# Performance work log

Measured on AMD Instinct MI355X. Metric: run time of the kernel, lower is better.

Reference implementation:

```python
import jax, jax.numpy as jnp
import numpy as np
import math

D = 128
LAMBDA_INIT = 0.8 - 0.6 * math.exp(-0.3 * 1)  # depth=1


def _clin(xr, xi, wr, wi, br, bi):
    # complex linear: (xr + i xi) @ (wr + i wi)^T + (br + i bi)
    o_r = jnp.einsum('bhsd,od->bhso', xr, wr) - jnp.einsum('bhsd,od->bhso', xi, wi) + br
    o_i = jnp.einsum('bhsd,od->bhso', xr, wi) + jnp.einsum('bhsd,od->bhso', xi, wr) + bi
    return o_r, o_i


def setup_inputs() -> dict:
    key = jax.random.key(0)
    ks = jax.random.split(key, 32)
    B, H, S = 1, 12, 1024
    shp = (B, H, S, D)
    inp = {}
    names = ['q_r', 'q_i', 'k_r', 'k_i', 'v_r', 'v_i', 'pe_q_r', 'pe_q_i', 'pe_k_r', 'pe_k_i']
    for i, n in enumerate(names):
        inp[n] = jax.random.normal(ks[i], shp, dtype=jnp.float32)
    std = 1.0 / math.sqrt(D)
    inp['qw_r'] = jax.random.normal(ks[10], (2 * D, D), jnp.float32) * std
    inp['qw_i'] = jax.random.normal(ks[11], (2 * D, D), jnp.float32) * std
    inp['qb_r'] = jnp.zeros((2 * D,), jnp.float32)
    inp['qb_i'] = jnp.zeros((2 * D,), jnp.float32)
    for j, p in enumerate(['k', 'v', 'g', 'o']):
        inp[p + 'w_r'] = jax.random.normal(ks[12 + 2 * j], (D, D), jnp.float32) * std
        inp[p + 'w_i'] = jax.random.normal(ks[13 + 2 * j], (D, D), jnp.float32) * std
        inp[p + 'b_r'] = jnp.zeros((D,), jnp.float32)
        inp[p + 'b_i'] = jnp.zeros((D,), jnp.float32)
    inp['lq1'] = jax.random.normal(ks[20], (D,), jnp.float32) * 0.1
    inp['lk1'] = jax.random.normal(ks[21], (D,), jnp.float32) * 0.1
    inp['lq2'] = jax.random.normal(ks[22], (D,), jnp.float32) * 0.1
    inp['lk2'] = jax.random.normal(ks[23], (D,), jnp.float32) * 0.1
    inp['sub_w'] = jnp.ones((2 * D,), jnp.float32)
    return inp


def _forward(q_r, q_i, k_r, k_i, v_r, v_i, pe_q_r, pe_q_i, pe_k_r, pe_k_i,
             qw_r, qw_i, qb_r, qb_i, kw_r, kw_i, kb_r, kb_i,
             vw_r, vw_i, vb_r, vb_i, gw_r, gw_i, gb_r, gb_i,
             ow_r, ow_i, ob_r, ob_i, lq1, lk1, lq2, lk2, sub_w):
    scale = D ** (-0.5)
    qp_r, qp_i = _clin(q_r, q_i, qw_r, qw_i, qb_r, qb_i)   # [B,H,S,2D]
    kp_r, kp_i = _clin(k_r, k_i, kw_r, kw_i, kb_r, kb_i)   # [B,H,S,D]
    vp_r, vp_i = _clin(v_r, v_i, vw_r, vw_i, vb_r, vb_i)
    qp_r = qp_r + jnp.concatenate([pe_q_r, pe_q_r], axis=-1)
    qp_i = qp_i + jnp.concatenate([pe_q_i, pe_q_i], axis=-1)
    kp_r = kp_r + pe_k_r
    kp_i = kp_i + pe_k_i
    q1_r, q2_r = jnp.split(qp_r, 2, axis=-1)
    q1_i, q2_i = jnp.split(qp_i, 2, axis=-1)

    def attn_w(qr, qi):
        s_r = jnp.einsum('bhqd,bhkd->bhqk', qr, kp_r) + jnp.einsum('bhqd,bhkd->bhqk', qi, kp_i)
        s_i = jnp.einsum('bhqd,bhkd->bhqk', qi, kp_r) - jnp.einsum('bhqd,bhkd->bhqk', qr, kp_i)
        mag = jnp.sqrt(s_r ** 2 + s_i ** 2 + 1e-8) * scale
        return jax.nn.softmax(mag.astype(jnp.float32), axis=-1).astype(s_r.dtype)

    w1 = attn_w(q1_r, q1_i)
    w2 = attn_w(q2_r, q2_i)
    a1_r = jnp.einsum('bhqk,bhkd->bhqd', w1, vp_r)
    a1_i = jnp.einsum('bhqk,bhkd->bhqd', w1, vp_i)
    a2_r = jnp.einsum('bhqk,bhkd->bhqd', w2, vp_r)
    a2_i = jnp.einsum('bhqk,bhkd->bhqd', w2, vp_i)
    cat_r = jnp.concatenate([a1_r, a2_r], axis=-1)
    cat_i = jnp.concatenate([a1_i, a2_i], axis=-1)
    rms = jnp.sqrt(jnp.mean(cat_r ** 2 + cat_i ** 2, axis=-1, keepdims=True) + 1e-5)
    cat_r = cat_r / rms * sub_w
    cat_i = cat_i / rms * sub_w
    a1_r, a2_r = jnp.split(cat_r, 2, axis=-1)
    a1_i, a2_i = jnp.split(cat_i, 2, axis=-1)
    lam1 = jnp.exp(jnp.sum(lq1 * lk1))
    lam2 = jnp.exp(jnp.sum(lq2 * lk2))
    lam = jax.nn.sigmoid(lam1 - lam2 + LAMBDA_INIT)
    out_r = a1_r - lam * a2_r
    out_i = a1_i - lam * a2_i
    g_r, g_i = _clin(q_r, q_i, gw_r, gw_i, gb_r, gb_i)
    out_r, out_i = g_r * out_r - g_i * out_i, g_r * out_i + g_i * out_r
    out_r, out_i = _clin(out_r, out_i, ow_r, ow_i, ob_r, ob_i)
    return out_r, out_i


def reference(q_r, q_i, k_r, k_i, v_r, v_i, pe_q_r, pe_q_i, pe_k_r, pe_k_i,
              qw_r, qw_i, qb_r, qb_i, kw_r, kw_i, kb_r, kb_i,
              vw_r, vw_i, vb_r, vb_i, gw_r, gw_i, gb_r, gb_i,
              ow_r, ow_i, ob_r, ob_i, lq1, lk1, lq2, lk2, sub_w):
    return _forward(q_r, q_i, k_r, k_i, v_r, v_i, pe_q_r, pe_q_i, pe_k_r, pe_k_i,
                    qw_r, qw_i, qb_r, qb_i, kw_r, kw_i, kb_r, kb_i,
                    vw_r, vw_i, vb_r, vb_i, gw_r, gw_i, gb_r, gb_i,
                    ow_r, ow_i, ob_r, ob_i, lq1, lk1, lq2, lk2, sub_w)
```

## Files before the change

kernel.cpp:

```cpp
#include <hip/hip_runtime.h>
#include <math.h>

#define H 12
#define S 1024
#define D 128
#define NROWS (H * S)

typedef __attribute__((ext_vector_type(8))) _Float16 f16x8;
typedef __attribute__((ext_vector_type(4))) float f32x4;
typedef __attribute__((ext_vector_type(4))) int i32x4;

__device__ __forceinline__ short f2h(float f) {
    _Float16 h = (_Float16)f;
    return __builtin_bit_cast(short, h);
}
__device__ __forceinline__ float h2f(short s) {
    return (float)__builtin_bit_cast(_Float16, s);
}
__device__ __forceinline__ f16x8 fneg8(f16x8 v) {
    i32x4 u = __builtin_bit_cast(i32x4, v);
    u ^= (int)0x80008000;
    return __builtin_bit_cast(f16x8, u);
}

#define WS_QP_R   0ULL
#define WS_QP_I   6291456ULL
#define WS_KP_R   12582912ULL
#define WS_KP_I   15728640ULL
#define WS_VPT_R  18874368ULL
#define WS_VPT_I  22020096ULL
#define WS_GP_R   25165824ULL
#define WS_GP_I   28311552ULL
#define WS_ACAT_R 31457280ULL
#define WS_ACAT_I 37748736ULL
#define WS_LAM    44040192ULL
#define WS_SC     44040448ULL
#define W16_PER_HEAD   4194304ULL
#define STAT_PER_HEAD  16384ULL

__global__ void lam_kernel(const float* __restrict__ lq1, const float* __restrict__ lk1,
                           const float* __restrict__ lq2, const float* __restrict__ lk2,
                           float* __restrict__ lam_out)
{
    int t = threadIdx.x;
    float p1 = lq1[t] * lk1[t];
    float p2 = lq2[t] * lk2[t];
    #pragma unroll
    for (int off = 32; off; off >>= 1) {
        p1 += __shfl_xor(p1, off);
        p2 += __shfl_xor(p2, off);
    }
    __shared__ float s1[2], s2[2];
    if ((t & 63) == 0) { s1[t >> 6] = p1; s2[t >> 6] = p2; }
    __syncthreads();
    if (t == 0) {
        float l1 = expf(s1[0] + s1[1]);
        float l2 = expf(s2[0] + s2[1]);
        float x = l1 - l2 + 0.3555090675909693f;
        lam_out[0] = 1.0f / (1.0f + expf(-x));
    }
}

__global__ __launch_bounds__(256) void proj_all(
    const float* __restrict__ q_r, const float* __restrict__ q_i,
    const float* __restrict__ k_r, const float* __restrict__ k_i,
    const float* __restrict__ v_r, const float* __restrict__ v_i,
    const float* __restrict__ pe_q_r, const float* __restrict__ pe_q_i,
    const float* __restrict__ pe_k_r, const float* __restrict__ pe_k_i,
    const float* __restrict__ qw_r, const float* __restrict__ qw_i,
    const float* __restrict__ qb_r, const float* __restrict__ qb_i,
    const float* __restrict__ kw_r, const float* __restrict__ kw_i,
// ... 153 lines not shown
        for (int ks = 0; ks < 64; ks += 32) {
            f16x8 bfr[2], bfi[2];
            #pragma unroll
            for (int j = 0; j < 2; ++j) {
                bfr[j] = *(const f16x8*)&Brs[(wn + j * 16 + fm) * 72 + ks + fq * 8];
                bfi[j] = *(const f16x8*)&Bis[(wn + j * 16 + fm) * 72 + ks + fq * 8];
            }
            #pragma unroll
            for (int i = 0; i < 2; ++i) {
                f16x8 a = *(const f16x8*)&As[(wm + i * 16 + fm) * 72 + ks + fq * 8];
                #pragma unroll
                for (int j = 0; j < 2; ++j) {
                    accr[i][j] = __builtin_amdgcn_mfma_f32_16x16x32_f16(a, bfr[j], accr[i][j], 0, 0, 0);
                    acci[i][j] = __builtin_amdgcn_mfma_f32_16x16x32_f16(a, bfi[j], acci[i][j], 0, 0, 0);
                }
            }
        }
    }
    #pragma unroll
    for (int i = 0; i < 2; ++i)
        #pragma unroll
        for (int j = 0; j < 2; ++j) {
            int colc = col0 + wn + j * 16 + fm;
            float bbr = br[colc], bbi = bi[colc];
            #pragma unroll
            for (int reg = 0; reg < 4; ++reg) {
                int rr = row0 + wm + i * 16 + fq * 4 + reg;
                outr[(size_t)rr * 128 + colc] = accr[i][j][reg] + bbr;
                outi[(size_t)rr * 128 + colc] = acci[i][j][reg] + bbi;
            }
        }
}

__global__ __launch_bounds__(256) void score_mfma(
    const short* __restrict__ qp_r, const short* __restrict__ qp_i,
    const short* __restrict__ kp_r, const short* __restrict__ kp_i,
    short* __restrict__ w16, int h0)
{
    __shared__ short Qr[64 * 72], Qi[64 * 72], Kt[128 * 72];
    const int t = threadIdx.x;
    const int hh = blockIdx.z >> 1, map = blockIdx.z & 1;
    const int h = h0 + hh;
    const int q0 = blockIdx.x * 64, c0 = blockIdx.y * 128;
    const int lane = t & 63, wid = t >> 6;
    const int wm = (wid >> 1) * 32, wn = (wid & 1) * 64;
    const int fm = lane & 15, fq = lane >> 4;
    f32x4 zero4 = {0.f, 0.f, 0.f, 0.f};
    f32x4 sr[2][4], si[2][4];
    #pragma unroll
    for (int i = 0; i < 2; ++i)
        #pragma unroll
        for (int j = 0; j < 4; ++j) { sr[i][j] = zero4; si[i][j] = zero4; }

    for (int kb = 0; kb < 2; ++kb) {
        const int kbase = map * 128 + kb * 64;
        __syncthreads();
        #pragma unroll
        for (int i = 0; i < 4; ++i) {
            int lin = i * 256 + t;
            int r = lin >> 4, k4 = (lin & 15) * 4;
            size_t qb = (size_t)(h * S + q0 + r) * 256 + kbase + k4;
            *(short4*)&Qr[r * 72 + k4] = *(const short4*)&qp_r[qb];
            *(short4*)&Qi[r * 72 + k4] = *(const short4*)&qp_i[qb];
        }
        #pragma unroll
        for (int i = 0; i < 8; ++i) {
            int lin = i * 256 + t;
            int r = lin >> 4, k4 = (lin & 15) * 4;
            *(short4*)&Kt[r * 72 + k4] =
                *(const short4*)&kp_r[(size_t)(h * S + c0 + r) * 128 + kb * 64 + k4];
        }
        __syncthreads();
        f16x8 aR[2][2], aI[2][2];
        #pragma unroll
        for (int ks = 0; ks < 2; ++ks)
            #pragma unroll
            for (int i = 0; i < 2; ++i) {
                int ao = (wm + i * 16 + fm) * 72 + ks * 32 + fq * 8;
                aR[ks][i] = *(const f16x8*)&Qr[ao];
                aI[ks][i] = *(const f16x8*)&Qi[ao];
            }
        #pragma unroll
        for (int ks = 0; ks < 2; ++ks) {
            f16x8 b[4];
            #pragma unroll
            for (int j = 0; j < 4; ++j)
                b[j] = *(const f16x8*)&Kt[(wn + j * 16 + fm) * 72 + ks * 32 + fq * 8];
            #pragma unroll
            for (int i = 0; i < 2; ++i)
                #pragma unroll
                for (int j = 0; j < 4; ++j) {
                    sr[i][j] = __builtin_amdgcn_mfma_f32_16x16x32_f16(aR[ks][i], b[j], sr[i][j], 0, 0, 0);
                    si[i][j] = __builtin_amdgcn_mfma_f32_16x16x32_f16(aI[ks][i], b[j], si[i][j], 0, 0, 0);
                }
        }
        __syncthreads();
        #pragma unroll
        for (int i = 0; i < 8; ++i) {
            int lin = i * 256 + t;
            int r = lin >> 4, k4 = (lin & 15) * 4;
            *(short4*)&Kt[r * 72 + k4] =
                *(const short4*)&kp_i[(size_t)(h * S + c0 + r) * 128 + kb * 64 + k4];
        }
        __syncthreads();
        #pragma unroll
        for (int ks = 0; ks < 2; ++ks) {
            f16x8 b[4];
            #pragma unroll
            for (int j = 0; j < 4; ++j)
                b[j] = *(const f16x8*)&Kt[(wn + j * 16 + fm) * 72 + ks * 32 + fq * 8];
            f16x8 nR0 = fneg8(aR[ks][0]), nR1 = fneg8(aR[ks][1]);
            #pragma unroll
            for (int j = 0; j < 4; ++j) {
                sr[0][j] = __builtin_amdgcn_mfma_f32_16x16x32_f16(aI[ks][0], b[j], sr[0][j], 0, 0, 0);
                si[0][j] = __builtin_amdgcn_mfma_f32_16x16x32_f16(nR0, b[j], si[0][j], 0, 0, 0);
                sr[1][j] = __builtin_amdgcn_mfma_f32_16x16x32_f16(aI[ks][1], b[j], sr[1][j], 0, 0, 0);
                si[1][j] = __builtin_amdgcn_mfma_f32_16x16x32_f16(nR1, b[j], si[1][j], 0, 0, 0);
            }
        }
    }
    const float scale = 0.08838834764831845f;
    #pragma unroll
    for (int i = 0; i < 2; ++i)
        #pragma unroll
        for (int j = 0; j < 4; ++j) {
            int kcol = c0 + wn + j * 16 + fm;
            #pragma unroll
            for (int reg = 0; reg < 4; ++reg) {
                int q = q0 + wm + i * 16 + fq * 4 + reg;
                float r1 = sr[i][j][reg], I1 = si[i][j][reg];
                float m1 = sqrtf(fmaf(r1, r1, fmaf(I1, I1, 1e-8f))) * scale;
                w16[(((size_t)hh * 2 + map) * S + q) * S + kcol] = f2h(m1);
            }
        }
}

__global__ __launch_bounds__(256) void smstats(const short* __restrict__ w16,
                                               float2* __restrict__ stats)
{
    const short* row = w16 + (size_t)blockIdx.x * S;
    int t = threadIdx.x;
    short4 s = ((const short4*)row)[t];
    float f0 = h2f(s.x), f1 = h2f(s.y), f2v = h2f(s.z), f3 = h2f(s.w);
    float m = fmaxf(fmaxf(f0, f1), fmaxf(f2v, f3));
    #pragma unroll
    for (int off = 32; off; off >>= 1) m = fmaxf(m, __shfl_xor(m, off));
    __shared__ float redm[4], reds[4];
    int w = t >> 6;
    if ((t & 63) == 0) redm[w] = m;
    __syncthreads();
    m = fmaxf(fmaxf(redm[0], redm[1]), fmaxf(redm[2], redm[3]));
    float ssum = __expf(f0 - m) + __expf(f1 - m) + __expf(f2v - m) + __expf(f3 - m);
    #pragma unroll
    for (int off = 32; off; off >>= 1) ssum += __shfl_xor(ssum, off);
    if ((t & 63) == 0) reds[w] = ssum;
    __syncthreads();
    if (t == 0) {
        float total = reds[0] + reds[1] + reds[2] + reds[3];
        stats[blockIdx.x] = make_float2(m, 1.0f / total);
    }
}

__global__ __launch_bounds__(256) void av_mfma(
    const short* __restrict__ w16, const float2* __restrict__ stats,
    const short* __restrict__ vpT_r, const short* __restrict__ vpT_i,
    short* __restrict__ acat_r, short* __restrict__ acat_i, int h0)
{
    __shared__ short W1[32 * 72], W2[32 * 72], Vc[128 * 72];
    const int t = threadIdx.x;
    const int hh = blockIdx.z, h = h0 + hh;
    const int comp = blockIdx.y;
    const int q0 = blockIdx.x * 32;
    const short* vpT = comp ? vpT_i : vpT_r;
    short* acat = comp ? acat_i : acat_r;
    const float2* st1 = stats + ((size_t)hh * 2 + 0) * S;
    const float2* st2 = stats + ((size_t)hh * 2 + 1) * S;
    const int lane = t & 63, wid = t >> 6;
    const int wm = (wid >> 1) * 16, wn = (wid & 1) * 64;
    const int fm = lane & 15, fq = lane >> 4;
    f32x4 zero4 = {0.f, 0.f, 0.f, 0.f};
    f32x4 a1[4], a2[4];
    #pragma unroll
    for (int j = 0; j < 4; ++j) { a1[j] = zero4; a2[j] = zero4; }

    for (int k0 = 0; k0 < S; k0 += 64) {
        __syncthreads();
        #pragma unroll
        for (int it = 0; it < 2; ++it) {
            int lin = it * 256 + t;
            int r = lin >> 4, k4 = (lin & 15) * 4;
            float2 s1v = st1[q0 + r];
            float2 s2v = st2[q0 + r];
            short4 m1 = *(const short4*)&w16[(((size_t)hh * 2 + 0) * S + q0 + r) * S + k0 + k4];
            short4 m2 = *(const short4*)&w16[(((size_t)hh * 2 + 1) * S + q0 + r) * S + k0 + k4];
            *(short4*)&W1[r * 72 + k4] = make_short4(
                f2h(__expf(h2f(m1.x) - s1v.x) * s1v.y), f2h(__expf(h2f(m1.y) - s1v.x) * s1v.y),
                f2h(__expf(h2f(m1.z) - s1v.x) * s1v.y), f2h(__expf(h2f(m1.w) - s1v.x) * s1v.y));
            *(short4*)&W2[r * 72 + k4] = make_short4(
                f2h(__expf(h2f(m2.x) - s2v.x) * s2v.y), f2h(__expf(h2f(m2.y) - s2v.x) * s2v.y),
                f2h(__expf(h2f(m2.z) - s2v.x) * s2v.y), f2h(__expf(h2f(m2.w) - s2v.x) * s2v.y));
        }
        #pragma unroll
        for (int it = 0; it < 8; ++it) {
            int lin = it * 256 + t;
            int dd = lin >> 4, k4 = (lin & 15) * 4;
            *(short4*)&Vc[dd * 72 + k4] = *(const short4*)&vpT[(size_t)(h * 128 + dd) * 1024 + k0 + k4];
        }
        __syncthreads();
        #pragma unroll
        for (int ks = 0; ks < 64; ks += 32) {
            f16x8 b[4];
            #pragma unroll
            for (int j = 0; j < 4; ++j)
                b[j] = *(const f16x8*)&Vc[(wn + j * 16 + fm) * 72 + ks + fq * 8];
            int wo = (wm + fm) * 72 + ks + fq * 8;
            f16x8 w1f = *(const f16x8*)&W1[wo];
            f16x8 w2f = *(const f16x8*)&W2[wo];
            #pragma unroll
            for (int j = 0; j < 4; ++j) {
                a1[j] = __builtin_amdgcn_mfma_f32_16x16x32_f16(w1f, b[j], a1[j], 0, 0, 0);
                a2[j] = __builtin_amdgcn_mfma_f32_16x16x32_f16(w2f, b[j], a2[j], 0, 0, 0);
            }
        }
    }
    #pragma unroll
    for (int j = 0; j < 4; ++j) {
        int d = wn + j * 16 + fm;
        #pragma unroll
        for (int reg = 0; reg < 4; ++reg) {
            int q = q0 + wm + fq * 4 + reg;
            size_t rowb = (size_t)(h * S + q) * 256;
            acat[rowb + d]       = f2h(a1[j][reg]);
            acat[rowb + 128 + d] = f2h(a2[j][reg]);
        }
    }
}

__global__ __launch_bounds__(256) void rmsgate_kernel(
    const short* __restrict__ acat_r, const short* __restrict__ acat_i,
    const float* __restrict__ sub_w, const float* __restrict__ lam_ptr,
    short* __restrict__ gp_r, short* __restrict__ gp_i)
{
    int row = blockIdx.x;
    int t = threadIdx.x;
    float ar = h2f(acat_r[(size_t)row * 256 + t]);
    float ai = h2f(acat_i[(size_t)row * 256 + t]);
    float ss = fmaf(ar, ar, ai * ai);
    #pragma unroll
    for (int off = 32; off; off >>= 1) ss += __shfl_xor(ss, off);
    __shared__ float red[4];
    if ((t & 63) == 0) red[t >> 6] = ss;
    __syncthreads();
    float total = red[0] + red[1] + red[2] + red[3];
    float inv_rms = 1.0f / sqrtf(total * (1.0f / 256.0f) + 1e-5f);
    float sw = sub_w[t];
    __shared__ float Cr[256], Ci[256];
    Cr[t] = ar * inv_rms * sw;
    Ci[t] = ai * inv_rms * sw;
    __syncthreads();
    if (t < 128) {
        float lam = lam_ptr[0];
        float o_r = Cr[t] - lam * Cr[t + 128];
        float o_i = Ci[t] - lam * Ci[t + 128];
        float gr = h2f(gp_r[(size_t)row * 128 + t]);
        float gi = h2f(gp_i[(size_t)row * 128 + t]);
        gp_r[(size_t)row * 128 + t] = f2h(gr * o_r - gi * o_i);
        gp_i[(size_t)row * 128 + t] = f2h(gr * o_i + gi * o_r);
    }
}

extern "C" void kernel_launch(void* const* d_in, const int* in_sizes, int n_in,
                              void* d_out, int out_size, void* d_ws, size_t ws_size,
                              hipStream_t stream)
{
    (void)in_sizes; (void)n_in; (void)out_size;
    const float* q_r    = (const float*)d_in[0];
    const float* q_i    = (const float*)d_in[1];
    const float* k_r    = (const float*)d_in[2];
    const float* k_i    = (const float*)d_in[3];
    const float* v_r    = (const float*)d_in[4];
    const float* v_i    = (const float*)d_in[5];
    const float* pe_q_r = (const float*)d_in[6];
    const float* pe_q_i = (const float*)d_in[7];
    const float* pe_k_r = (const float*)d_in[8];
    const float* pe_k_i = (const float*)d_in[9];
    const float* qw_r   = (const float*)d_in[10];
    const float* qw_i   = (const float*)d_in[11];
    const float* qb_r   = (const float*)d_in[12];
    const float* qb_i   = (const float*)d_in[13];
    const float* kw_r   = (const float*)d_in[14];
    const float* kw_i   = (const float*)d_in[15];
    const float* kb_r   = (const float*)d_in[16];
    const float* kb_i   = (const float*)d_in[17];
    const float* vw_r   = (const float*)d_in[18];
    const float* vw_i   = (const float*)d_in[19];
    const float* vb_r   = (const float*)d_in[20];
    const float* vb_i   = (const float*)d_in[21];
    const float* gw_r   = (const float*)d_in[22];
    const float* gw_i   = (const float*)d_in[23];
    const float* gb_r   = (const float*)d_in[24];
    const float* gb_i   = (const float*)d_in[25];
    const float* ow_r   = (const float*)d_in[26];
    const float* ow_i   = (const float*)d_in[27];
    const float* ob_r   = (const float*)d_in[28];
    const float* ob_i   = (const float*)d_in[29];
    const float* lq1    = (const float*)d_in[30];
    const float* lk1    = (const float*)d_in[31];
    const float* lq2    = (const float*)d_in[32];
    const float* lk2    = (const float*)d_in[33];
    const float* sub_w  = (const float*)d_in[34];

    char* ws = (char*)d_ws;
    short* qp_r   = (short*)(ws + WS_QP_R);
    short* qp_i   = (short*)(ws + WS_QP_I);
    short* kp_r   = (short*)(ws + WS_KP_R);
    short* kp_i   = (short*)(ws + WS_KP_I);
    short* vpT_r  = (short*)(ws + WS_VPT_R);
    short* vpT_i  = (short*)(ws + WS_VPT_I);
    short* gp_r   = (short*)(ws + WS_GP_R);
    short* gp_i   = (short*)(ws + WS_GP_I);
    short* acat_r = (short*)(ws + WS_ACAT_R);
    short* acat_i = (short*)(ws + WS_ACAT_I);
    float* lam    = (float*)(ws + WS_LAM);
    short* w16    = (short*)(ws + WS_SC);

    float* out_r = (float*)d_out;
    float* out_i = out_r + (size_t)NROWS * D;

    size_t avail = ws_size > WS_SC ? ws_size - WS_SC : 0;
    int nh_chunk = (int)(avail / (W16_PER_HEAD + STAT_PER_HEAD));
    if (nh_chunk < 1) nh_chunk = 1;
    if (nh_chunk > H) nh_chunk = H;
    float2* stats = (float2*)(ws + WS_SC + (size_t)nh_chunk * W16_PER_HEAD);

    lam_kernel<<<1, 128, 0, stream>>>(lq1, lk1, lq2, lk2, lam);

    proj_all<<<dim3(192, 10), 256, 0, stream>>>(
        q_r, q_i, k_r, k_i, v_r, v_i, pe_q_r, pe_q_i, pe_k_r, pe_k_i,
        qw_r, qw_i, qb_r, qb_i, kw_r, kw_i, kb_r, kb_i,
        vw_r, vw_i, vb_r, vb_i, gw_r, gw_i, gb_r, gb_i,
        qp_r, qp_i, kp_r, kp_i, vpT_r, vpT_i, gp_r, gp_i);

    for (int h0 = 0; h0 < H; h0 += nh_chunk) {
        int nhh = (H - h0 < nh_chunk) ? (H - h0) : nh_chunk;
        score_mfma<<<dim3(16, 8, nhh * 2), 256, 0, stream>>>(qp_r, qp_i, kp_r, kp_i, w16, h0);
        smstats<<<nhh * 2 * S, 256, 0, stream>>>(w16, stats);
        av_mfma<<<dim3(32, 2, nhh), 256, 0, stream>>>(w16, stats, vpT_r, vpT_i, acat_r, acat_i, h0);
    }

    rmsgate_kernel<<<NROWS, 256, 0, stream>>>(acat_r, acat_i, sub_w, lam, gp_r, gp_i);

    oproj_mfma<<<dim3(192, 2), 256, 0, stream>>>(gp_r, gp_i, ow_r, ow_i, ob_r, ob_i, out_r, out_i);
}
```

Measured before the change: 296.7 us.

## Fuse score, softmax stats and AV into a flash-style attention kernel

```diff
diff --git a/kernel.cpp b/kernel.cpp
--- a/kernel.cpp
+++ b/kernel.cpp
@@ -34,9 +34,6 @@
 #define WS_ACAT_R 31457280ULL
 #define WS_ACAT_I 37748736ULL
 #define WS_LAM    44040192ULL
-#define WS_SC     44040448ULL
-#define W16_PER_HEAD   4194304ULL
-#define STAT_PER_HEAD  16384ULL
 
 __global__ void lam_kernel(const float* __restrict__ lq1, const float* __restrict__ lk1,
                            const float* __restrict__ lq2, const float* __restrict__ lk2,
@@ -256,206 +253,143 @@
         }
 }
 
-__global__ __launch_bounds__(256) void score_mfma(
+#define KI_OFF 8704
+#define VI_OFF 9216
+__global__ __launch_bounds__(128) void fused_attn(
     const short* __restrict__ qp_r, const short* __restrict__ qp_i,
     const short* __restrict__ kp_r, const short* __restrict__ kp_i,
-    short* __restrict__ w16, int h0)
+    const short* __restrict__ vpT_r, const short* __restrict__ vpT_i,
+    short* __restrict__ acat_r, short* __restrict__ acat_i)
 {
-    __shared__ short Qr[64 * 72], Qi[64 * 72], Kt[128 * 72];
+    __shared__ __align__(16) short KV[18432];
+    __shared__ __align__(16) short Pl[32 * 72];
     const int t = threadIdx.x;
-    const int hh = blockIdx.z >> 1, map = blockIdx.z & 1;
-    const int h = h0 + hh;
-    const int q0 = blockIdx.x * 64, c0 = blockIdx.y * 128;
     const int lane = t & 63, wid = t >> 6;
-    const int wm = (wid >> 1) * 32, wn = (wid & 1) * 64;
     const int fm = lane & 15, fq = lane >> 4;
+    const int q0 = blockIdx.x * 32;
+    const int map = blockIdx.y;
+    const int h = blockIdx.z;
+
+    f16x8 qR[4], qI[4];
+    {
+        size_t qrow = (size_t)(h * S + q0 + wid * 16 + fm) * 256 + map * 128;
+        #pragma unroll
+        for (int ks = 0; ks < 4; ++ks) {
+            qR[ks] = *(const f16x8*)&qp_r[qrow + ks * 32 + fq * 8];
+            qI[ks] = *(const f16x8*)&qp_i[qrow + ks * 32 + fq * 8];
+        }
+    }
     f32x4 zero4 = {0.f, 0.f, 0.f, 0.f};
-    f32x4 sr[2][4], si[2][4];
-    #pragma unroll
-    for (int i = 0; i < 2; ++i)
-        #pragma unroll
-        for (int j = 0; j < 4; ++j) { sr[i][j] = zero4; si[i][j] = zero4; }
-
-    for (int kb = 0; kb < 2; ++kb) {
-        const int kbase = map * 128 + kb * 64;
-        __syncthreads();
-        #pragma unroll
-        for (int i = 0; i < 4; ++i) {
-            int lin = i * 256 + t;
-            int r = lin >> 4, k4 = (lin & 15) * 4;
-            size_t qb = (size_t)(h * S + q0 + r) * 256 + kbase + k4;
-            *(short4*)&Qr[r * 72 + k4] = *(const short4*)&qp_r[qb];
-            *(short4*)&Qi[r * 72 + k4] = *(const short4*)&qp_i[qb];
-        }
-        #pragma unroll
-        for (int i = 0; i < 8; ++i) {
-            int lin = i * 256 + t;
-            int r = lin >> 4, k4 = (lin & 15) * 4;
-            *(short4*)&Kt[r * 72 + k4] =
-                *(const short4*)&kp_r[(size_t)(h * S + c0 + r) * 128 + kb * 64 + k4];
-        }
-        __syncthreads();
-        f16x8 aR[2][2], aI[2][2];
-        #pragma unroll
-        for (int ks = 0; ks < 2; ++ks)
-            #pragma unroll
-            for (int i = 0; i < 2; ++i) {
-                int ao = (wm + i * 16 + fm) * 72 + ks * 32 + fq * 8;
-                aR[ks][i] = *(const f16x8*)&Qr[ao];
-                aI[ks][i] = *(const f16x8*)&Qi[ao];
-            }
-        #pragma unroll
-        for (int ks = 0; ks < 2; ++ks) {
-            f16x8 b[4];
-            #pragma unroll
-            for (int j = 0; j < 4; ++j)
-                b[j] = *(const f16x8*)&Kt[(wn + j * 16 + fm) * 72 + ks * 32 + fq * 8];
-            #pragma unroll
-            for (int i = 0; i < 2; ++i)
+    f32x4 accO[2][8];
+    #pragma unroll
+    for (int c = 0; c < 2; ++c)
+        #pragma unroll
+        for (int dj = 0; dj < 8; ++dj) accO[c][dj] = zero4;
+    float m_run[4], l_run[4];
+    #pragma unroll
+    for (int reg = 0; reg < 4; ++reg) { m_run[reg] = -3.0e38f; l_run[reg] = 0.f; }
+
+    const float scale = 0.08838834764831845f;
+
+    for (int k0 = 0; k0 < S; k0 += 64) {
+        __syncthreads();
+        #pragma unroll
+        for (int it = 0; it < 8; ++it) {
+            int lin = it * 128 + t;
+            int r = lin >> 4, c8 = (lin & 15) * 8;
+            size_t src = (size_t)(h * S + k0 + r) * 128 + c8;
+            *(i32x4*)&KV[r * 136 + c8]          = *(const i32x4*)&kp_r[src];
+            *(i32x4*)&KV[KI_OFF + r * 136 + c8] = *(const i32x4*)&kp_i[src];
+        }
+        __syncthreads();
+        f32x4 sr[4], si[4];
+        #pragma unroll
+        for (int j = 0; j < 4; ++j) { sr[j] = zero4; si[j] = zero4; }
+        #pragma unroll
+        for (int ks = 0; ks < 4; ++ks) {
+            f16x8 aR = qR[ks], aI = qI[ks], nR = fneg8(qR[ks]);
+            #pragma unroll
+            for (int j = 0; j < 4; ++j) {
+                int bo = (j * 16 + fm) * 136 + ks * 32 + fq * 8;
+                f16x8 bR = *(const f16x8*)&KV[bo];
+                f16x8 bI = *(const f16x8*)&KV[KI_OFF + bo];
+                sr[j] = __builtin_amdgcn_mfma_f32_16x16x32_f16(aR, bR, sr[j], 0, 0, 0);
+                si[j] = __builtin_amdgcn_mfma_f32_16x16x32_f16(aI, bR, si[j], 0, 0, 0);
+                sr[j] = __builtin_amdgcn_mfma_f32_16x16x32_f16(aI, bI, sr[j], 0, 0, 0);
+                si[j] = __builtin_amdgcn_mfma_f32_16x16x32_f16(nR, bI, si[j], 0, 0, 0);
+            }
+        }
+        float p[4][4];
+        #pragma unroll
+        for (int j = 0; j < 4; ++j)
+            #pragma unroll
+            for (int reg = 0; reg < 4; ++reg)
+                p[j][reg] = sqrtf(fmaf(sr[j][reg], sr[j][reg],
+                                       fmaf(si[j][reg], si[j][reg], 1e-8f))) * scale;
+        float sc[4];
+        #pragma unroll
+        for (int reg = 0; reg < 4; ++reg) {
+            float mx = fmaxf(fmaxf(p[0][reg], p[1][reg]), fmaxf(p[2][reg], p[3][reg]));
+            #pragma unroll
+            for (int off = 1; off < 16; off <<= 1) mx = fmaxf(mx, __shfl_xor(mx, off));
+            float mnew = fmaxf(m_run[reg], mx);
+            sc[reg] = __expf(m_run[reg] - mnew);
+            m_run[reg] = mnew;
+            float ssum = 0.f;
+            #pragma unroll
+            for (int j = 0; j < 4; ++j) {
+                p[j][reg] = __expf(p[j][reg] - mnew);
+                ssum += p[j][reg];
+            }
+            #pragma unroll
+            for (int off = 1; off < 16; off <<= 1) ssum += __shfl_xor(ssum, off);
+            l_run[reg] = l_run[reg] * sc[reg] + ssum;
+        }
+        #pragma unroll
+        for (int c = 0; c < 2; ++c)
+            #pragma unroll
+            for (int dj = 0; dj < 8; ++dj)
                 #pragma unroll
-                for (int j = 0; j < 4; ++j) {
-                    sr[i][j] = __builtin_amdgcn_mfma_f32_16x16x32_f16(aR[ks][i], b[j], sr[i][j], 0, 0, 0);
-                    si[i][j] = __builtin_amdgcn_mfma_f32_16x16x32_f16(aI[ks][i], b[j], si[i][j], 0, 0, 0);
-                }
-        }
-        __syncthreads();
-        #pragma unroll
-        for (int i = 0; i < 8; ++i) {
-            int lin = i * 256 + t;
-            int r = lin >> 4, k4 = (lin & 15) * 4;
-            *(short4*)&Kt[r * 72 + k4] =
-                *(const short4*)&kp_i[(size_t)(h * S + c0 + r) * 128 + kb * 64 + k4];
-        }
-        __syncthreads();
-        #pragma unroll
-        for (int ks = 0; ks < 2; ++ks) {
-            f16x8 b[4];
-            #pragma unroll
-            for (int j = 0; j < 4; ++j)
-                b[j] = *(const f16x8*)&Kt[(wn + j * 16 + fm) * 72 + ks * 32 + fq * 8];
-            f16x8 nR0 = fneg8(aR[ks][0]), nR1 = fneg8(aR[ks][1]);
-            #pragma unroll
-            for (int j = 0; j < 4; ++j) {
-                sr[0][j] = __builtin_amdgcn_mfma_f32_16x16x32_f16(aI[ks][0], b[j], sr[0][j], 0, 0, 0);
-                si[0][j] = __builtin_amdgcn_mfma_f32_16x16x32_f16(nR0, b[j], si[0][j], 0, 0, 0);
-                sr[1][j] = __builtin_amdgcn_mfma_f32_16x16x32_f16(aI[ks][1], b[j], sr[1][j], 0, 0, 0);
-                si[1][j] = __builtin_amdgcn_mfma_f32_16x16x32_f16(nR1, b[j], si[1][j], 0, 0, 0);
-            }
-        }
-    }
-    const float scale = 0.08838834764831845f;
-    #pragma unroll
-    for (int i = 0; i < 2; ++i)
-        #pragma unroll
-        for (int j = 0; j < 4; ++j) {
-            int kcol = c0 + wn + j * 16 + fm;
-            #pragma unroll
-            for (int reg = 0; reg < 4; ++reg) {
-                int q = q0 + wm + i * 16 + fq * 4 + reg;
-                float r1 = sr[i][j][reg], I1 = si[i][j][reg];
-                float m1 = sqrtf(fmaf(r1, r1, fmaf(I1, I1, 1e-8f))) * scale;
-                w16[(((size_t)hh * 2 + map) * S + q) * S + kcol] = f2h(m1);
-            }
-        }
-}
-
-__global__ __launch_bounds__(256) void smstats(const short* __restrict__ w16,
-                                               float2* __restrict__ stats)
-{
-    const short* row = w16 + (size_t)blockIdx.x * S;
-    int t = threadIdx.x;
-    short4 s = ((const short4*)row)[t];
-    float f0 = h2f(s.x), f1 = h2f(s.y), f2v = h2f(s.z), f3 = h2f(s.w);
-    float m = fmaxf(fmaxf(f0, f1), fmaxf(f2v, f3));
-    #pragma unroll
-    for (int off = 32; off; off >>= 1) m = fmaxf(m, __shfl_xor(m, off));
-    __shared__ float redm[4], reds[4];
-    int w = t >> 6;
-    if ((t & 63) == 0) redm[w] = m;
-    __syncthreads();
-    m = fmaxf(fmaxf(redm[0], redm[1]), fmaxf(redm[2], redm[3]));
-    float ssum = __expf(f0 - m) + __expf(f1 - m) + __expf(f2v - m) + __expf(f3 - m);
-    #pragma unroll
-    for (int off = 32; off; off >>= 1) ssum += __shfl_xor(ssum, off);
-    if ((t & 63) == 0) reds[w] = ssum;
-    __syncthreads();
-    if (t == 0) {
-        float total = reds[0] + reds[1] + reds[2] + reds[3];
-        stats[blockIdx.x] = make_float2(m, 1.0f / total);
-    }
-}
-
-__global__ __launch_bounds__(256) void av_mfma(
-    const short* __restrict__ w16, const float2* __restrict__ stats,
-    const short* __restrict__ vpT_r, const short* __restrict__ vpT_i,
-    short* __restrict__ acat_r, short* __restrict__ acat_i, int h0)
-{
-    __shared__ short W1[32 * 72], W2[32 * 72], Vc[128 * 72];
-    const int t = threadIdx.x;
-    const int hh = blockIdx.z, h = h0 + hh;
-    const int comp = blockIdx.y;
-    const int q0 = blockIdx.x * 32;
-    const short* vpT = comp ? vpT_i : vpT_r;
-    short* acat = comp ? acat_i : acat_r;
-    const float2* st1 = stats + ((size_t)hh * 2 + 0) * S;
-    const float2* st2 = stats + ((size_t)hh * 2 + 1) * S;
-    const int lane = t & 63, wid = t >> 6;
-    const int wm = (wid >> 1) * 16, wn = (wid & 1) * 64;
-    const int fm = lane & 15, fq = lane >> 4;
-    f32x4 zero4 = {0.f, 0.f, 0.f, 0.f};
-    f32x4 a1[4], a2[4];
-    #pragma unroll
-    for (int j = 0; j < 4; ++j) { a1[j] = zero4; a2[j] = zero4; }
-
-    for (int k0 = 0; k0 < S; k0 += 64) {
-        __syncthreads();
-        #pragma unroll
-        for (int it = 0; it < 2; ++it) {
-            int lin = it * 256 + t;
-            int r = lin >> 4, k4 = (lin & 15) * 4;
-            float2 s1v = st1[q0 + r];
-            float2 s2v = st2[q0 + r];
-            short4 m1 = *(const short4*)&w16[(((size_t)hh * 2 + 0) * S + q0 + r) * S + k0 + k4];
-            short4 m2 = *(const short4*)&w16[(((size_t)hh * 2 + 1) * S + q0 + r) * S + k0 + k4];
-            *(short4*)&W1[r * 72 + k4] = make_short4(
-                f2h(__expf(h2f(m1.x) - s1v.x) * s1v.y), f2h(__expf(h2f(m1.y) - s1v.x) * s1v.y),
-                f2h(__expf(h2f(m1.z) - s1v.x) * s1v.y), f2h(__expf(h2f(m1.w) - s1v.x) * s1v.y));
-            *(short4*)&W2[r * 72 + k4] = make_short4(
-                f2h(__expf(h2f(m2.x) - s2v.x) * s2v.y), f2h(__expf(h2f(m2.y) - s2v.x) * s2v.y),
-                f2h(__expf(h2f(m2.z) - s2v.x) * s2v.y), f2h(__expf(h2f(m2.w) - s2v.x) * s2v.y));
-        }
+                for (int reg = 0; reg < 4; ++reg)
+                    accO[c][dj][reg] *= sc[reg];
+        __syncthreads();
         #pragma unroll
         for (int it = 0; it < 8; ++it) {
-            int lin = it * 256 + t;
-            int dd = lin >> 4, k4 = (lin & 15) * 4;
-            *(short4*)&Vc[dd * 72 + k4] = *(const short4*)&vpT[(size_t)(h * 128 + dd) * 1024 + k0 + k4];
-        }
-        __syncthreads();
-        #pragma unroll
-        for (int ks = 0; ks < 64; ks += 32) {
-            f16x8 b[4];
-            #pragma unroll
-            for (int j = 0; j < 4; ++j)
-                b[j] = *(const f16x8*)&Vc[(wn + j * 16 + fm) * 72 + ks + fq * 8];
-            int wo = (wm + fm) * 72 + ks + fq * 8;
-            f16x8 w1f = *(const f16x8*)&W1[wo];
-            f16x8 w2f = *(const f16x8*)&W2[wo];
-            #pragma unroll
-            for (int j = 0; j < 4; ++j) {
-                a1[j] = __builtin_amdgcn_mfma_f32_16x16x32_f16(w1f, b[j], a1[j], 0, 0, 0);
-                a2[j] = __builtin_amdgcn_mfma_f32_16x16x32_f16(w2f, b[j], a2[j], 0, 0, 0);
-            }
-        }
-    }
-    #pragma unroll
-    for (int j = 0; j < 4; ++j) {
-        int d = wn + j * 16 + fm;
-        #pragma unroll
-        for (int reg = 0; reg < 4; ++reg) {
-            int q = q0 + wm + fq * 4 + reg;
-            size_t rowb = (size_t)(h * S + q) * 256;
-            acat[rowb + d]       = f2h(a1[j][reg]);
-            acat[rowb + 128 + d] = f2h(a2[j][reg]);
+            int lin = it * 128 + t;
+            int dd = lin >> 3, c8 = (lin & 7) * 8;
+            size_t src = (size_t)(h * 128 + dd) * 1024 + k0 + c8;
+            *(i32x4*)&KV[dd * 72 + c8]          = *(const i32x4*)&vpT_r[src];
+            *(i32x4*)&KV[VI_OFF + dd * 72 + c8] = *(const i32x4*)&vpT_i[src];
+        }
+        #pragma unroll
+        for (int j = 0; j < 4; ++j)
+            #pragma unroll
+            for (int reg = 0; reg < 4; ++reg)
+                Pl[(wid * 16 + fq * 4 + reg) * 72 + j * 16 + fm] = f2h(p[j][reg]);
+        __syncthreads();
+        #pragma unroll
+        for (int ks2 = 0; ks2 < 2; ++ks2) {
+            f16x8 w8 = *(const f16x8*)&Pl[(wid * 16 + fm) * 72 + ks2 * 32 + fq * 8];
+            #pragma unroll
+            for (int dj = 0; dj < 8; ++dj) {
+                int vo = (dj * 16 + fm) * 72 + ks2 * 32 + fq * 8;
+                f16x8 br = *(const f16x8*)&KV[vo];
+                f16x8 bi = *(const f16x8*)&KV[VI_OFF + vo];
+                accO[0][dj] = __builtin_amdgcn_mfma_f32_16x16x32_f16(w8, br, accO[0][dj], 0, 0, 0);
+                accO[1][dj] = __builtin_amdgcn_mfma_f32_16x16x32_f16(w8, bi, accO[1][dj], 0, 0, 0);
+            }
+        }
+    }
+    #pragma unroll
+    for (int reg = 0; reg < 4; ++reg) {
+        float invl = 1.0f / l_run[reg];
+        int q = q0 + wid * 16 + fq * 4 + reg;
+        size_t rowb = (size_t)(h * S + q) * 256 + map * 128;
+        #pragma unroll
+        for (int dj = 0; dj < 8; ++dj) {
+            int d = dj * 16 + fm;
+            acat_r[rowb + d] = f2h(accO[0][dj][reg] * invl);
+            acat_i[rowb + d] = f2h(accO[1][dj][reg] * invl);
         }
     }
 }
@@ -497,7 +431,7 @@
                               void* d_out, int out_size, void* d_ws, size_t ws_size,
                               hipStream_t stream)
 {
-    (void)in_sizes; (void)n_in; (void)out_size;
+    (void)in_sizes; (void)n_in; (void)out_size; (void)ws_size;
     const float* q_r    = (const float*)d_in[0];
     const float* q_i    = (const float*)d_in[1];
     const float* k_r    = (const float*)d_in[2];
@@ -546,16 +480,9 @@
     short* acat_r = (short*)(ws + WS_ACAT_R);
     short* acat_i = (short*)(ws + WS_ACAT_I);
     float* lam    = (float*)(ws + WS_LAM);
-    short* w16    = (short*)(ws + WS_SC);
 
     float* out_r = (float*)d_out;
     float* out_i = out_r + (size_t)NROWS * D;
-
-    size_t avail = ws_size > WS_SC ? ws_size - WS_SC : 0;
-    int nh_chunk = (int)(avail / (W16_PER_HEAD + STAT_PER_HEAD));
-    if (nh_chunk < 1) nh_chunk = 1;
-    if (nh_chunk > H) nh_chunk = H;
-    float2* stats = (float2*)(ws + WS_SC + (size_t)nh_chunk * W16_PER_HEAD);
 
     lam_kernel<<<1, 128, 0, stream>>>(lq1, lk1, lq2, lk2, lam);
 
@@ -565,12 +492,8 @@
         vw_r, vw_i, vb_r, vb_i, gw_r, gw_i, gb_r, gb_i,
         qp_r, qp_i, kp_r, kp_i, vpT_r, vpT_i, gp_r, gp_i);
 
-    for (int h0 = 0; h0 < H; h0 += nh_chunk) {
-        int nhh = (H - h0 < nh_chunk) ? (H - h0) : nh_chunk;
-        score_mfma<<<dim3(16, 8, nhh * 2), 256, 0, stream>>>(qp_r, qp_i, kp_r, kp_i, w16, h0);
-        smstats<<<nhh * 2 * S, 256, 0, stream>>>(w16, stats);
-        av_mfma<<<dim3(32, 2, nhh), 256, 0, stream>>>(w16, stats, vpT_r, vpT_i, acat_r, acat_i, h0);
-    }
+    fused_attn<<<dim3(32, 2, H), 128, 0, stream>>>(
+        qp_r, qp_i, kp_r, kp_i, vpT_r, vpT_i, acat_r, acat_i);
 
     rmsgate_kernel<<<NROWS, 256, 0, stream>>>(acat_r, acat_i, sub_w, lam, gp_r, gp_i);
 
```

After: 575.3 us. +93.9%, slower.

## Fuse softmax stats into AV kernel via online softmax; load Q fragments directly

Applied to the files above, without the earlier changes.

```diff
diff --git a/kernel.cpp b/kernel.cpp
--- a/kernel.cpp
+++ b/kernel.cpp
@@ -36,7 +36,6 @@
 #define WS_LAM    44040192ULL
 #define WS_SC     44040448ULL
 #define W16_PER_HEAD   4194304ULL
-#define STAT_PER_HEAD  16384ULL
 
 __global__ void lam_kernel(const float* __restrict__ lq1, const float* __restrict__ lk1,
                            const float* __restrict__ lq2, const float* __restrict__ lk2,
@@ -261,7 +260,7 @@
     const short* __restrict__ kp_r, const short* __restrict__ kp_i,
     short* __restrict__ w16, int h0)
 {
-    __shared__ short Qr[64 * 72], Qi[64 * 72], Kt[128 * 72];
+    __shared__ short Kr[128 * 72], Ki[128 * 72];
     const int t = threadIdx.x;
     const int hh = blockIdx.z >> 1, map = blockIdx.z & 1;
     const int h = h0 + hh;
@@ -277,69 +276,42 @@
         for (int j = 0; j < 4; ++j) { sr[i][j] = zero4; si[i][j] = zero4; }
 
     for (int kb = 0; kb < 2; ++kb) {
-        const int kbase = map * 128 + kb * 64;
         __syncthreads();
         #pragma unroll
         for (int i = 0; i < 4; ++i) {
             int lin = i * 256 + t;
-            int r = lin >> 4, k4 = (lin & 15) * 4;
-            size_t qb = (size_t)(h * S + q0 + r) * 256 + kbase + k4;
-            *(short4*)&Qr[r * 72 + k4] = *(const short4*)&qp_r[qb];
-            *(short4*)&Qi[r * 72 + k4] = *(const short4*)&qp_i[qb];
-        }
-        #pragma unroll
-        for (int i = 0; i < 8; ++i) {
-            int lin = i * 256 + t;
-            int r = lin >> 4, k4 = (lin & 15) * 4;
-            *(short4*)&Kt[r * 72 + k4] =
-                *(const short4*)&kp_r[(size_t)(h * S + c0 + r) * 128 + kb * 64 + k4];
-        }
-        __syncthreads();
+            int r = lin >> 3, c8 = (lin & 7) * 8;
+            size_t src = (size_t)(h * S + c0 + r) * 128 + kb * 64 + c8;
+            *(i32x4*)&Kr[r * 72 + c8] = *(const i32x4*)&kp_r[src];
+            *(i32x4*)&Ki[r * 72 + c8] = *(const i32x4*)&kp_i[src];
+        }
         f16x8 aR[2][2], aI[2][2];
         #pragma unroll
         for (int ks = 0; ks < 2; ++ks)
             #pragma unroll
             for (int i = 0; i < 2; ++i) {
-                int ao = (wm + i * 16 + fm) * 72 + ks * 32 + fq * 8;
-                aR[ks][i] = *(const f16x8*)&Qr[ao];
-                aI[ks][i] = *(const f16x8*)&Qi[ao];
-            }
+                size_t qa = (size_t)(h * S + q0 + wm + i * 16 + fm) * 256
+                            + map * 128 + kb * 64 + ks * 32 + fq * 8;
+                aR[ks][i] = *(const f16x8*)&qp_r[qa];
+                aI[ks][i] = *(const f16x8*)&qp_i[qa];
+            }
+        __syncthreads();
         #pragma unroll
         for (int ks = 0; ks < 2; ++ks) {
-            f16x8 b[4];
-            #pragma unroll
-            for (int j = 0; j < 4; ++j)
-                b[j] = *(const f16x8*)&Kt[(wn + j * 16 + fm) * 72 + ks * 32 + fq * 8];
-            #pragma unroll
-            for (int i = 0; i < 2; ++i)
-                #pragma unroll
-                for (int j = 0; j < 4; ++j) {
-                    sr[i][j] = __builtin_amdgcn_mfma_f32_16x16x32_f16(aR[ks][i], b[j], sr[i][j], 0, 0, 0);
-                    si[i][j] = __builtin_amdgcn_mfma_f32_16x16x32_f16(aI[ks][i], b[j], si[i][j], 0, 0, 0);
-                }
-        }
-        __syncthreads();
-        #pragma unroll
-        for (int i = 0; i < 8; ++i) {
-            int lin = i * 256 + t;
-            int r = lin >> 4, k4 = (lin & 15) * 4;
-            *(short4*)&Kt[r * 72 + k4] =
-                *(const short4*)&kp_i[(size_t)(h * S + c0 + r) * 128 + kb * 64 + k4];
-        }
-        __syncthreads();
-        #pragma unroll
-        for (int ks = 0; ks < 2; ++ks) {
-            f16x8 b[4];
-            #pragma unroll
-            for (int j = 0; j < 4; ++j)
-                b[j] = *(const f16x8*)&Kt[(wn + j * 16 + fm) * 72 + ks * 32 + fq * 8];
             f16x8 nR0 = fneg8(aR[ks][0]), nR1 = fneg8(aR[ks][1]);
             #pragma unroll
             for (int j = 0; j < 4; ++j) {
-                sr[0][j] = __builtin_amdgcn_mfma_f32_16x16x32_f16(aI[ks][0], b[j], sr[0][j], 0, 0, 0);
-                si[0][j] = __builtin_amdgcn_mfma_f32_16x16x32_f16(nR0, b[j], si[0][j], 0, 0, 0);
-                sr[1][j] = __builtin_amdgcn_mfma_f32_16x16x32_f16(aI[ks][1], b[j], sr[1][j], 0, 0, 0);
-                si[1][j] = __builtin_amdgcn_mfma_f32_16x16x32_f16(nR1, b[j], si[1][j], 0, 0, 0);
+                int bo = (wn + j * 16 + fm) * 72 + ks * 32 + fq * 8;
+                f16x8 bR = *(const f16x8*)&Kr[bo];
+                f16x8 bI = *(const f16x8*)&Ki[bo];
+                sr[0][j] = __builtin_amdgcn_mfma_f32_16x16x32_f16(aR[ks][0], bR, sr[0][j], 0, 0, 0);
+                si[0][j] = __builtin_amdgcn_mfma_f32_16x16x32_f16(aI[ks][0], bR, si[0][j], 0, 0, 0);
+                sr[0][j] = __builtin_amdgcn_mfma_f32_16x16x32_f16(aI[ks][0], bI, sr[0][j], 0, 0, 0);
+                si[0][j] = __builtin_amdgcn_mfma_f32_16x16x32_f16(nR0, bI, si[0][j], 0, 0, 0);
+                sr[1][j] = __builtin_amdgcn_mfma_f32_16x16x32_f16(aR[ks][1], bR, sr[1][j], 0, 0, 0);
+                si[1][j] = __builtin_amdgcn_mfma_f32_16x16x32_f16(aI[ks][1], bR, si[1][j], 0, 0, 0);
+                sr[1][j] = __builtin_amdgcn_mfma_f32_16x16x32_f16(aI[ks][1], bI, sr[1][j], 0, 0, 0);
+                si[1][j] = __builtin_amdgcn_mfma_f32_16x16x32_f16(nR1, bI, si[1][j], 0, 0, 0);
             }
         }
     }
@@ -359,46 +331,19 @@
         }
 }
 
-__global__ __launch_bounds__(256) void smstats(const short* __restrict__ w16,
-                                               float2* __restrict__ stats)
-{
-    const short* row = w16 + (size_t)blockIdx.x * S;
-    int t = threadIdx.x;
-    short4 s = ((const short4*)row)[t];
-    float f0 = h2f(s.x), f1 = h2f(s.y), f2v = h2f(s.z), f3 = h2f(s.w);
-    float m = fmaxf(fmaxf(f0, f1), fmaxf(f2v, f3));
-    #pragma unroll
-    for (int off = 32; off; off >>= 1) m = fmaxf(m, __shfl_xor(m, off));
-    __shared__ float redm[4], reds[4];
-    int w = t >> 6;
-    if ((t & 63) == 0) redm[w] = m;
-    __syncthreads();
-    m = fmaxf(fmaxf(redm[0], redm[1]), fmaxf(redm[2], redm[3]));
-    float ssum = __expf(f0 - m) + __expf(f1 - m) + __expf(f2v - m) + __expf(f3 - m);
-    #pragma unroll
-    for (int off = 32; off; off >>= 1) ssum += __shfl_xor(ssum, off);
-    if ((t & 63) == 0) reds[w] = ssum;
-    __syncthreads();
-    if (t == 0) {
-        float total = reds[0] + reds[1] + reds[2] + reds[3];
-        stats[blockIdx.x] = make_float2(m, 1.0f / total);
-    }
-}
-
-__global__ __launch_bounds__(256) void av_mfma(
-    const short* __restrict__ w16, const float2* __restrict__ stats,
+__global__ __launch_bounds__(256) void av_online(
+    const short* __restrict__ w16,
     const short* __restrict__ vpT_r, const short* __restrict__ vpT_i,
     short* __restrict__ acat_r, short* __restrict__ acat_i, int h0)
 {
     __shared__ short W1[32 * 72], W2[32 * 72], Vc[128 * 72];
+    __shared__ float mrun[2][32], lrun[2][32], scL[2][32];
     const int t = threadIdx.x;
     const int hh = blockIdx.z, h = h0 + hh;
     const int comp = blockIdx.y;
     const int q0 = blockIdx.x * 32;
     const short* vpT = comp ? vpT_i : vpT_r;
     short* acat = comp ? acat_i : acat_r;
-    const float2* st1 = stats + ((size_t)hh * 2 + 0) * S;
-    const float2* st2 = stats + ((size_t)hh * 2 + 1) * S;
     const int lane = t & 63, wid = t >> 6;
     const int wm = (wid >> 1) * 16, wn = (wid & 1) * 64;
     const int fm = lane & 15, fq = lane >> 4;
@@ -406,6 +351,10 @@
     f32x4 a1[4], a2[4];
     #pragma unroll
     for (int j = 0; j < 4; ++j) { a1[j] = zero4; a2[j] = zero4; }
+    if (t < 32) {
+        mrun[0][t] = -3.0e38f; lrun[0][t] = 0.f;
+        mrun[1][t] = -3.0e38f; lrun[1][t] = 0.f;
+    }
 
     for (int k0 = 0; k0 < S; k0 += 64) {
         __syncthreads();
@@ -413,24 +362,61 @@
         for (int it = 0; it < 2; ++it) {
             int lin = it * 256 + t;
             int r = lin >> 4, k4 = (lin & 15) * 4;
-            float2 s1v = st1[q0 + r];
-            float2 s2v = st2[q0 + r];
             short4 m1 = *(const short4*)&w16[(((size_t)hh * 2 + 0) * S + q0 + r) * S + k0 + k4];
             short4 m2 = *(const short4*)&w16[(((size_t)hh * 2 + 1) * S + q0 + r) * S + k0 + k4];
-            *(short4*)&W1[r * 72 + k4] = make_short4(
-                f2h(__expf(h2f(m1.x) - s1v.x) * s1v.y), f2h(__expf(h2f(m1.y) - s1v.x) * s1v.y),
-                f2h(__expf(h2f(m1.z) - s1v.x) * s1v.y), f2h(__expf(h2f(m1.w) - s1v.x) * s1v.y));
-            *(short4*)&W2[r * 72 + k4] = make_short4(
-                f2h(__expf(h2f(m2.x) - s2v.x) * s2v.y), f2h(__expf(h2f(m2.y) - s2v.x) * s2v.y),
-                f2h(__expf(h2f(m2.z) - s2v.x) * s2v.y), f2h(__expf(h2f(m2.w) - s2v.x) * s2v.y));
+            float f10 = h2f(m1.x), f11 = h2f(m1.y), f12 = h2f(m1.z), f13 = h2f(m1.w);
+            float f20 = h2f(m2.x), f21 = h2f(m2.y), f22 = h2f(m2.z), f23 = h2f(m2.w);
+            float mx1 = fmaxf(fmaxf(f10, f11), fmaxf(f12, f13));
+            #pragma unroll
+            for (int off = 1; off < 16; off <<= 1) mx1 = fmaxf(mx1, __shfl_xor(mx1, off));
+            float mo1 = mrun[0][r];
+            float mn1 = fmaxf(mo1, mx1);
+            float e10 = __expf(f10 - mn1), e11 = __expf(f11 - mn1);
+            float e12 = __expf(f12 - mn1), e13 = __expf(f13 - mn1);
+            float s1 = e10 + e11 + e12 + e13;
+            #pragma unroll
+            for (int off = 1; off < 16; off <<= 1) s1 += __shfl_xor(s1, off);
+            float mx2 = fmaxf(fmaxf(f20, f21), fmaxf(f22, f23));
+            #pragma unroll
+            for (int off = 1; off < 16; off <<= 1) mx2 = fmaxf(mx2, __shfl_xor(mx2, off));
+            float mo2 = mrun[1][r];
+            float mn2 = fmaxf(mo2, mx2);
+            float e20 = __expf(f20 - mn2), e21 = __expf(f21 - mn2);
+            float e22 = __expf(f22 - mn2), e23 = __expf(f23 - mn2);
+            float s2 = e20 + e21 + e22 + e23;
+            #pragma unroll
+            for (int off = 1; off < 16; off <<= 1) s2 += __shfl_xor(s2, off);
+            if ((t & 15) == 0) {
+                float sc1 = __expf(mo1 - mn1);
+                mrun[0][r] = mn1; scL[0][r] = sc1;
+                lrun[0][r] = lrun[0][r] * sc1 + s1;
+                float sc2 = __expf(mo2 - mn2);
+                mrun[1][r] = mn2; scL[1][r] = sc2;
+                lrun[1][r] = lrun[1][r] * sc2 + s2;
+            }
+            *(short4*)&W1[r * 72 + k4] = make_short4(f2h(e10), f2h(e11), f2h(e12), f2h(e13));
+            *(short4*)&W2[r * 72 + k4] = make_short4(f2h(e20), f2h(e21), f2h(e22), f2h(e23));
         }
         #pragma unroll
         for (int it = 0; it < 8; ++it) {
             int lin = it * 256 + t;
-            int dd = lin >> 4, k4 = (lin & 15) * 4;
-            *(short4*)&Vc[dd * 72 + k4] = *(const short4*)&vpT[(size_t)(h * 128 + dd) * 1024 + k0 + k4];
-        }
-        __syncthreads();
+            int dd = lin >> 4, k4v = (lin & 15) * 4;
+            *(short4*)&Vc[dd * 72 + k4v] = *(const short4*)&vpT[(size_t)(h * 128 + dd) * 1024 + k0 + k4v];
+        }
+        __syncthreads();
+        float s1v[4], s2v[4];
+        #pragma unroll
+        for (int reg = 0; reg < 4; ++reg) {
+            s1v[reg] = scL[0][wm + fq * 4 + reg];
+            s2v[reg] = scL[1][wm + fq * 4 + reg];
+        }
+        #pragma unroll
+        for (int j = 0; j < 4; ++j)
+            #pragma unroll
+            for (int reg = 0; reg < 4; ++reg) {
+                a1[j][reg] *= s1v[reg];
+                a2[j][reg] *= s2v[reg];
+            }
         #pragma unroll
         for (int ks = 0; ks < 64; ks += 32) {
             f16x8 b[4];
@@ -447,6 +433,12 @@
             }
         }
     }
+    float invl1[4], invl2[4];
+    #pragma unroll
+    for (int reg = 0; reg < 4; ++reg) {
+        invl1[reg] = 1.0f / lrun[0][wm + fq * 4 + reg];
+        invl2[reg] = 1.0f / lrun[1][wm + fq * 4 + reg];
+    }
     #pragma unroll
     for (int j = 0; j < 4; ++j) {
         int d = wn + j * 16 + fm;
@@ -454,8 +446,8 @@
         for (int reg = 0; reg < 4; ++reg) {
             int q = q0 + wm + fq * 4 + reg;
             size_t rowb = (size_t)(h * S + q) * 256;
-            acat[rowb + d]       = f2h(a1[j][reg]);
-            acat[rowb + 128 + d] = f2h(a2[j][reg]);
+            acat[rowb + d]       = f2h(a1[j][reg] * invl1[reg]);
+            acat[rowb + 128 + d] = f2h(a2[j][reg] * invl2[reg]);
         }
     }
 }
@@ -552,10 +544,9 @@
     float* out_i = out_r + (size_t)NROWS * D;
 
     size_t avail = ws_size > WS_SC ? ws_size - WS_SC : 0;
-    int nh_chunk = (int)(avail / (W16_PER_HEAD + STAT_PER_HEAD));
+    int nh_chunk = (int)(avail / W16_PER_HEAD);
     if (nh_chunk < 1) nh_chunk = 1;
     if (nh_chunk > H) nh_chunk = H;
-    float2* stats = (float2*)(ws + WS_SC + (size_t)nh_chunk * W16_PER_HEAD);
 
     lam_kernel<<<1, 128, 0, stream>>>(lq1, lk1, lq2, lk2, lam);
 
@@ -568,8 +559,7 @@
     for (int h0 = 0; h0 < H; h0 += nh_chunk) {
         int nhh = (H - h0 < nh_chunk) ? (H - h0) : nh_chunk;
         score_mfma<<<dim3(16, 8, nhh * 2), 256, 0, stream>>>(qp_r, qp_i, kp_r, kp_i, w16, h0);
-        smstats<<<nhh * 2 * S, 256, 0, stream>>>(w16, stats);
-        av_mfma<<<dim3(32, 2, nhh), 256, 0, stream>>>(w16, stats, vpT_r, vpT_i, acat_r, acat_i, h0);
+        av_online<<<dim3(32, 2, nhh), 256, 0, stream>>>(w16, vpT_r, vpT_i, acat_r, acat_i, h0);
     }
 
     rmsgate_kernel<<<NROWS, 256, 0, stream>>>(acat_r, acat_i, sub_w, lam, gp_r, gp_i);
```

After: 345.8 us. +16.6%, slower.

## Load Q fragments directly from global and stage K real/imag together in LDS

Applied to the files above, without the earlier changes.

```diff
diff --git a/kernel.cpp b/kernel.cpp
--- a/kernel.cpp
+++ b/kernel.cpp
@@ -261,7 +261,7 @@
     const short* __restrict__ kp_r, const short* __restrict__ kp_i,
     short* __restrict__ w16, int h0)
 {
-    __shared__ short Qr[64 * 72], Qi[64 * 72], Kt[128 * 72];
+    __shared__ short Kr[128 * 72], Ki[128 * 72];
     const int t = threadIdx.x;
     const int hh = blockIdx.z >> 1, map = blockIdx.z & 1;
     const int h = h0 + hh;
@@ -277,69 +277,42 @@
         for (int j = 0; j < 4; ++j) { sr[i][j] = zero4; si[i][j] = zero4; }
 
     for (int kb = 0; kb < 2; ++kb) {
-        const int kbase = map * 128 + kb * 64;
         __syncthreads();
         #pragma unroll
         for (int i = 0; i < 4; ++i) {
             int lin = i * 256 + t;
-            int r = lin >> 4, k4 = (lin & 15) * 4;
-            size_t qb = (size_t)(h * S + q0 + r) * 256 + kbase + k4;
-            *(short4*)&Qr[r * 72 + k4] = *(const short4*)&qp_r[qb];
-            *(short4*)&Qi[r * 72 + k4] = *(const short4*)&qp_i[qb];
-        }
-        #pragma unroll
-        for (int i = 0; i < 8; ++i) {
-            int lin = i * 256 + t;
-            int r = lin >> 4, k4 = (lin & 15) * 4;
-            *(short4*)&Kt[r * 72 + k4] =
-                *(const short4*)&kp_r[(size_t)(h * S + c0 + r) * 128 + kb * 64 + k4];
-        }
-        __syncthreads();
+            int r = lin >> 3, c8 = (lin & 7) * 8;
+            size_t src = (size_t)(h * S + c0 + r) * 128 + kb * 64 + c8;
+            *(i32x4*)&Kr[r * 72 + c8] = *(const i32x4*)&kp_r[src];
+            *(i32x4*)&Ki[r * 72 + c8] = *(const i32x4*)&kp_i[src];
+        }
         f16x8 aR[2][2], aI[2][2];
         #pragma unroll
         for (int ks = 0; ks < 2; ++ks)
             #pragma unroll
             for (int i = 0; i < 2; ++i) {
-                int ao = (wm + i * 16 + fm) * 72 + ks * 32 + fq * 8;
-                aR[ks][i] = *(const f16x8*)&Qr[ao];
-                aI[ks][i] = *(const f16x8*)&Qi[ao];
-            }
+                size_t qa = (size_t)(h * S + q0 + wm + i * 16 + fm) * 256
+                            + map * 128 + kb * 64 + ks * 32 + fq * 8;
+                aR[ks][i] = *(const f16x8*)&qp_r[qa];
+                aI[ks][i] = *(const f16x8*)&qp_i[qa];
+            }
+        __syncthreads();
         #pragma unroll
         for (int ks = 0; ks < 2; ++ks) {
-            f16x8 b[4];
-            #pragma unroll
-            for (int j = 0; j < 4; ++j)
-                b[j] = *(const f16x8*)&Kt[(wn + j * 16 + fm) * 72 + ks * 32 + fq * 8];
-            #pragma unroll
-            for (int i = 0; i < 2; ++i)
-                #pragma unroll
-                for (int j = 0; j < 4; ++j) {
-                    sr[i][j] = __builtin_amdgcn_mfma_f32_16x16x32_f16(aR[ks][i], b[j], sr[i][j], 0, 0, 0);
-                    si[i][j] = __builtin_amdgcn_mfma_f32_16x16x32_f16(aI[ks][i], b[j], si[i][j], 0, 0, 0);
-                }
-        }
-        __syncthreads();
-        #pragma unroll
-        for (int i = 0; i < 8; ++i) {
-            int lin = i * 256 + t;
-            int r = lin >> 4, k4 = (lin & 15) * 4;
-            *(short4*)&Kt[r * 72 + k4] =
-                *(const short4*)&kp_i[(size_t)(h * S + c0 + r) * 128 + kb * 64 + k4];
-        }
-        __syncthreads();
-        #pragma unroll
-        for (int ks = 0; ks < 2; ++ks) {
-            f16x8 b[4];
-            #pragma unroll
-            for (int j = 0; j < 4; ++j)
-                b[j] = *(const f16x8*)&Kt[(wn + j * 16 + fm) * 72 + ks * 32 + fq * 8];
             f16x8 nR0 = fneg8(aR[ks][0]), nR1 = fneg8(aR[ks][1]);
             #pragma unroll
             for (int j = 0; j < 4; ++j) {
-                sr[0][j] = __builtin_amdgcn_mfma_f32_16x16x32_f16(aI[ks][0], b[j], sr[0][j], 0, 0, 0);
-                si[0][j] = __builtin_amdgcn_mfma_f32_16x16x32_f16(nR0, b[j], si[0][j], 0, 0, 0);
-                sr[1][j] = __builtin_amdgcn_mfma_f32_16x16x32_f16(aI[ks][1], b[j], sr[1][j], 0, 0, 0);
-                si[1][j] = __builtin_amdgcn_mfma_f32_16x16x32_f16(nR1, b[j], si[1][j], 0, 0, 0);
+                int bo = (wn + j * 16 + fm) * 72 + ks * 32 + fq * 8;
+                f16x8 bR = *(const f16x8*)&Kr[bo];
+                f16x8 bI = *(const f16x8*)&Ki[bo];
+                sr[0][j] = __builtin_amdgcn_mfma_f32_16x16x32_f16(aR[ks][0], bR, sr[0][j], 0, 0, 0);
+                si[0][j] = __builtin_amdgcn_mfma_f32_16x16x32_f16(aI[ks][0], bR, si[0][j], 0, 0, 0);
+                sr[0][j] = __builtin_amdgcn_mfma_f32_16x16x32_f16(aI[ks][0], bI, sr[0][j], 0, 0, 0);
+                si[0][j] = __builtin_amdgcn_mfma_f32_16x16x32_f16(nR0, bI, si[0][j], 0, 0, 0);
+                sr[1][j] = __builtin_amdgcn_mfma_f32_16x16x32_f16(aR[ks][1], bR, sr[1][j], 0, 0, 0);
+                si[1][j] = __builtin_amdgcn_mfma_f32_16x16x32_f16(aI[ks][1], bR, si[1][j], 0, 0, 0);
+                sr[1][j] = __builtin_amdgcn_mfma_f32_16x16x32_f16(aI[ks][1], bI, sr[1][j], 0, 0, 0);
+                si[1][j] = __builtin_amdgcn_mfma_f32_16x16x32_f16(nR1, bI, si[1][j], 0, 0, 0);
             }
         }
     }
```

Result: slower. 317.4 us (+7.0%).
